# Kernel tuning notes

Measured on AMD Instinct MI355X. Metric: run time of the kernel, lower is better.

The kernel has to match this reference:

```python
import jax, jax.numpy as jnp
import numpy as np

P = 40000       # points
DEG = 16        # neighbors per point (bs_slice rows are full: count == DEG)
E = P * DEG     # total edges
CI = 16         # in channels
CO = 16         # out channels


def setup_inputs() -> dict:
    key = jax.random.key(0)
    k1, k2, k3, k4 = jax.random.split(key, 4)
    features = jax.random.normal(k1, (P, CI), dtype=jnp.float32)
    radii = jax.random.normal(k2, (E, 3), dtype=jnp.float32)
    W = jax.random.normal(k3, (3, CO, CI), dtype=jnp.float32) * 0.1
    # bs_slice: [P, 1+DEG]; col 0 = neighbor count (DEG), cols 1: = neighbor idx
    nbrs = jax.random.randint(k4, (P, DEG), 0, P, dtype=jnp.int32)
    counts = jnp.full((P, 1), DEG, dtype=jnp.int32)
    bs_slice = jnp.concatenate([counts, nbrs], axis=1)
    return {"features": features, "radii": radii, "W": W, "bs_slice": bs_slice}


def reference(features, radii, W, bs_slice):
    # Edge list: torch loop consumes kernels sequentially, point-major.
    points_num = features.shape[0]
    deg = bs_slice.shape[1] - 1
    fa = jnp.repeat(jnp.arange(points_num, dtype=jnp.int32), deg)   # [E] dest point
    fb = bs_slice[:, 1:].reshape(-1)                                # [E] src point
    # Kernel(radii): linear radial map -> per-edge kernel [E, CO, CI]
    kernels = jnp.einsum('ed,doi->eoi', radii, W)
    # message per edge: kernels[e] @ features[fb[e]]
    msg = jnp.einsum('eoi,ei->eo', kernels, features[fb])
    # scatter-add into destination points
    out = jax.ops.segment_sum(msg, fa, num_segments=points_num)     # [P, CO]
    return out
```

## Files before the change

kernel.cpp:

```cpp
#include <hip/hip_runtime.h>


__global__ __launch_bounds__(256) void k_conv(const float* __restrict__ feat,
                                              const float* __restrict__ radii,
                                              const float* __restrict__ W,
                                              const int* __restrict__ bs,
                                              float* __restrict__ out,
                                              int P) {
    __shared__ float s_Wt[3][16][16];
    __shared__ int   s_nbr[16][16];
    __shared__ float s_r[16][48];
    __shared__ float s_h[16][48];

    const int tid = threadIdx.x;
    const int pbase = blockIdx.x * 16;
    const int lp = tid >> 4;
    const int li = tid & 15;

    for (int t = tid; t < 768; t += 256) {
        const int d = t >> 8;
        const int o = (t >> 4) & 15;
        const int i = t & 15;
        s_Wt[d][i][o] = W[t];
    }
    {
        const int p = pbase + lp;
        s_nbr[lp][li] = (p < P) ? bs[(size_t)p * 17 + 1 + li] : 0;
    }
    {
        float* srf = &s_r[0][0];
        const size_t lim = (size_t)P * 48;
        for (int t = tid; t < 768; t += 256) {
            const size_t gi = (size_t)pbase * 48 + t;
            srf[t] = (gi < lim) ? radii[gi] : 0.f;
        }
    }
    __syncthreads();

    float h0 = 0.f, h1 = 0.f, h2 = 0.f;
#pragma unroll
    for (int n = 0; n < 16; ++n) {
        const int src = s_nbr[lp][n];
        const float fv = feat[(size_t)src * 16 + li];
        h0 += s_r[lp][n * 3 + 0] * fv;
        h1 += s_r[lp][n * 3 + 1] * fv;
        h2 += s_r[lp][n * 3 + 2] * fv;
    }
    s_h[lp][li]      = h0;
    s_h[lp][16 + li] = h1;
    s_h[lp][32 + li] = h2;
    __syncthreads();

    const int p = pbase + lp;
    if (p >= P) return;

    float acc = 0.f;
#pragma unroll
    for (int d = 0; d < 3; ++d) {
#pragma unroll
        for (int i = 0; i < 16; ++i) {
            acc += s_Wt[d][i][li] * s_h[lp][d * 16 + i];
        }
    }
    out[(size_t)p * 16 + li] = acc;
}

extern "C" void kernel_launch(void* const* d_in, const int* in_sizes, int n_in,
                              void* d_out, int out_size, void* d_ws, size_t ws_size,
                              hipStream_t stream) {
    const float* feat  = (const float*)d_in[0];
    const float* radii = (const float*)d_in[1];
    const float* W     = (const float*)d_in[2];
    const int*   bs    = (const int*)d_in[3];
    float* out = (float*)d_out;

    const int P = in_sizes[0] / 16;
    const int grid = (P + 15) / 16;
    k_conv<<<grid, 256, 0, stream>>>(feat, radii, W, bs, out, P);
}
```

Baseline: 13.85 us.

## Remap to four threads per point with float4 gathers and shuffle reduction

Each block now handles 64 points instead of 16, with four threads per point. Each thread gathers float4 chunks of neighbor features and computes partial outputs over its slice of input channels. The partials are reduced across the four lanes with xor shuffles, which drops the second shared-memory stage and the extra barrier. The cost is more registers per thread (16 output accumulators plus 16 neighbor indices) and padded shared arrays.

```diff
diff --git a/kernel.cpp b/kernel.cpp
--- a/kernel.cpp
+++ b/kernel.cpp
@@ -7,62 +7,81 @@
                                               const int* __restrict__ bs,
                                               float* __restrict__ out,
                                               int P) {
-    __shared__ float s_Wt[3][16][16];
-    __shared__ int   s_nbr[16][16];
-    __shared__ float s_r[16][48];
-    __shared__ float s_h[16][48];
+    __shared__ float s_W[768];
+    __shared__ int   s_nbr[64][17];
+    __shared__ float s_r[64][49];
 
     const int tid = threadIdx.x;
-    const int pbase = blockIdx.x * 16;
-    const int lp = tid >> 4;
-    const int li = tid & 15;
+    const int pbase = blockIdx.x * 64;
+    const int lp = tid >> 2;
+    const int lq = tid & 3;
 
-    for (int t = tid; t < 768; t += 256) {
-        const int d = t >> 8;
-        const int o = (t >> 4) & 15;
-        const int i = t & 15;
-        s_Wt[d][i][o] = W[t];
+    if (tid < 192) {
+        reinterpret_cast<float4*>(s_W)[tid] = reinterpret_cast<const float4*>(W)[tid];
+    }
+    for (int t = tid; t < 1024; t += 256) {
+        const int l = t >> 4, n = t & 15;
+        const int p = pbase + l;
+        s_nbr[l][n] = (p < P) ? bs[(size_t)p * 17 + 1 + n] : 0;
     }
     {
-        const int p = pbase + lp;
-        s_nbr[lp][li] = (p < P) ? bs[(size_t)p * 17 + 1 + li] : 0;
-    }
-    {
-        float* srf = &s_r[0][0];
         const size_t lim = (size_t)P * 48;
-        for (int t = tid; t < 768; t += 256) {
+        for (int t = tid; t < 3072; t += 256) {
             const size_t gi = (size_t)pbase * 48 + t;
-            srf[t] = (gi < lim) ? radii[gi] : 0.f;
+            const int l = t / 48;
+            const int c = t - l * 48;
+            s_r[l][c] = (gi < lim) ? radii[gi] : 0.f;
         }
     }
     __syncthreads();
 
-    float h0 = 0.f, h1 = 0.f, h2 = 0.f;
+    int nb[16];
+#pragma unroll
+    for (int n = 0; n < 16; ++n) nb[n] = s_nbr[lp][n];
+
+    float4 h0 = {0.f, 0.f, 0.f, 0.f};
+    float4 h1 = {0.f, 0.f, 0.f, 0.f};
+    float4 h2 = {0.f, 0.f, 0.f, 0.f};
+    const float4* feat4 = reinterpret_cast<const float4*>(feat);
 #pragma unroll
     for (int n = 0; n < 16; ++n) {
-        const int src = s_nbr[lp][n];
-        const float fv = feat[(size_t)src * 16 + li];
-        h0 += s_r[lp][n * 3 + 0] * fv;
-        h1 += s_r[lp][n * 3 + 1] * fv;
-        h2 += s_r[lp][n * 3 + 2] * fv;
+        const float4 f = feat4[(size_t)nb[n] * 4 + lq];
+        const float r0 = s_r[lp][n * 3 + 0];
+        const float r1 = s_r[lp][n * 3 + 1];
+        const float r2 = s_r[lp][n * 3 + 2];
+        h0.x += r0 * f.x; h0.y += r0 * f.y; h0.z += r0 * f.z; h0.w += r0 * f.w;
+        h1.x += r1 * f.x; h1.y += r1 * f.y; h1.z += r1 * f.z; h1.w += r1 * f.w;
+        h2.x += r2 * f.x; h2.y += r2 * f.y; h2.z += r2 * f.z; h2.w += r2 * f.w;
     }
-    s_h[lp][li]      = h0;
-    s_h[lp][16 + li] = h1;
-    s_h[lp][32 + li] = h2;
-    __syncthreads();
+
+    const float4* sW4 = reinterpret_cast<const float4*>(s_W);
+    float po[16];
+#pragma unroll
+    for (int o = 0; o < 16; ++o) po[o] = 0.f;
+#pragma unroll
+    for (int d = 0; d < 3; ++d) {
+        const float4 hd = (d == 0) ? h0 : (d == 1) ? h1 : h2;
+#pragma unroll
+        for (int o = 0; o < 16; ++o) {
+            const float4 w = sW4[d * 64 + o * 4 + lq];
+            po[o] += w.x * hd.x + w.y * hd.y + w.z * hd.z + w.w * hd.w;
+        }
+    }
+#pragma unroll
+    for (int o = 0; o < 16; ++o) {
+        po[o] += __shfl_xor(po[o], 1, 64);
+        po[o] += __shfl_xor(po[o], 2, 64);
+    }
 
     const int p = pbase + lp;
-    if (p >= P) return;
-
-    float acc = 0.f;
-#pragma unroll
-    for (int d = 0; d < 3; ++d) {
-#pragma unroll
-        for (int i = 0; i < 16; ++i) {
-            acc += s_Wt[d][i][li] * s_h[lp][d * 16 + i];
-        }
+    if (p < P) {
+        float4 v;
+        if (lq == 0)      { v.x = po[0];  v.y = po[1];  v.z = po[2];  v.w = po[3];  }
+        else if (lq == 1) { v.x = po[4];  v.y = po[5];  v.z = po[6];  v.w = po[7];  }
+        else if (lq == 2) { v.x = po[8];  v.y = po[9];  v.z = po[10]; v.w = po[11]; }
+        else              { v.x = po[12]; v.y = po[13]; v.z = po[14]; v.w = po[15]; }
+        reinterpret_cast<float4*>(out)[(size_t)p * 4 + lq] = v;
     }
-    out[(size_t)p * 16 + li] = acc;
 }
 
 extern "C" void kernel_launch(void* const* d_in, const int* in_sizes, int n_in,
@@ -75,6 +94,6 @@
     float* out = (float*)d_out;
 
     const int P = in_sizes[0] / 16;
-    const int grid = (P + 15) / 16;
+    const int grid = (P + 63) / 64;
     k_conv<<<grid, 256, 0, stream>>>(feat, radii, W, bs, out, P);
 }
```

Measured after the change: 16.69 us. +20.6%, slower.
